# Kernel optimization log

Hardware: AMD Instinct MI355X
Metric: run time of the kernel (lower is better)

## Reference

```python
import jax, jax.numpy as jnp
import numpy as np

T, B, D, H = 1024, 64, 512, 512


def setup_inputs() -> dict:
    key = jax.random.key(0)
    ks = jax.random.split(key, 12)
    s_in = 1.0 / np.sqrt(D + H)  # torch Linear default init scale
    inp = {
        "inputs": jax.random.normal(ks[0], (T, B, D), dtype=jnp.float32),
        "Wf": jax.random.uniform(ks[1], (H, D + H), jnp.float32, -s_in, s_in),
        "bf": jax.random.uniform(ks[2], (H,), jnp.float32, -s_in, s_in),
        "Wi": jax.random.uniform(ks[3], (H, D + H), jnp.float32, -s_in, s_in),
        "bi": jax.random.uniform(ks[4], (H,), jnp.float32, -s_in, s_in),
        "Wg": jax.random.uniform(ks[5], (H, D + H), jnp.float32, -s_in, s_in),
        "bg": jax.random.uniform(ks[6], (H,), jnp.float32, -s_in, s_in),
        "Wo": jax.random.uniform(ks[7], (H, D + H), jnp.float32, -s_in, s_in),
        "bo": jax.random.uniform(ks[8], (H,), jnp.float32, -s_in, s_in),
        "q_scale": jnp.ones((H,), jnp.float32),
        "q_bias": jax.random.normal(ks[9], (H,), dtype=jnp.float32),
    }
    return inp


def reference(inputs, Wf, bf, Wi, bi, Wg, bg, Wo, bo, q_scale, q_bias):
    # Fuse the four gate projections into one GEMM: same math as 4 Linears.
    W_all = jnp.concatenate([Wf, Wi, Wg, Wo], axis=0)   # [4H, D+H]
    b_all = jnp.concatenate([bf, bi, bg, bo], axis=0)   # [4H]
    Bsz = inputs.shape[1]
    h0 = jnp.zeros((Bsz, H), inputs.dtype)
    c0 = jnp.zeros((Bsz, H), inputs.dtype)

    def qresc(a):
        return jnp.tanh(a * q_scale + q_bias)

    def step(carry, x):
        hx, cx = carry
        comb = jnp.concatenate([x, hx], axis=1)          # [B, D+H]
        z = comb @ W_all.T + b_all                       # [B, 4H]
        f, i, g, o = jnp.split(z, 4, axis=1)
        f = qresc(jax.nn.sigmoid(f))
        i = qresc(jax.nn.sigmoid(i))
        g = qresc(jnp.tanh(g))
        o = qresc(jax.nn.sigmoid(o))
        cx = f * cx + i * g
        hx = o * jnp.tanh(cx)
        return (hx, cx), hx

    (hx, cx), outputs = jax.lax.scan(step, (h0, c0), inputs)
    return outputs, hx, cx
```

## Files before the change

### kernel.cpp

```cpp
#include <hip/hip_runtime.h>


#define T_STEPS 1024
#define BATCH   64
#define DIM     512
#define HID     512
#define NGROUPS 4
#define BPG     64
#define BB      16
#define NBLOCKS 256

typedef __bf16 bf16_t;
typedef __bf16 bf16x8 __attribute__((ext_vector_type(8)));
typedef float  f32x4  __attribute__((ext_vector_type(4)));

#define WS_FLAGS_OFF 0
#define WS_WB_OFF    4096
#define WB_BYTES     ((size_t)64*32*1024*2)
#define WS_XB_OFF    (WS_WB_OFF + WB_BYTES)
#define XB_BYTES     ((size_t)T_STEPS*BATCH*DIM*2)
#define HBUF_BYTES   ((size_t)(T_STEPS+1)*BATCH*HID*2)
#define WS_FULL      (WS_XB_OFF + XB_BYTES + HBUF_BYTES)
#define WS_MIN       (WS_XB_OFF + HBUF_BYTES)

#define SMEM_BYTES 99328
#define LROW_W 1032
#define LROW_H 520

__device__ __forceinline__ unsigned pk2(float lo, float hi) {
  unsigned a = (unsigned)__builtin_bit_cast(unsigned short, (bf16_t)lo);
  unsigned b = (unsigned)__builtin_bit_cast(unsigned short, (bf16_t)hi);
  return (b << 16) | a;
}

__global__ void prep_kernel(const float* __restrict__ Wf, const float* __restrict__ Wi,
                            const float* __restrict__ Wg, const float* __restrict__ Wo,
                            const float* __restrict__ X,
                            unsigned* __restrict__ flags, unsigned* __restrict__ Wb,
                            unsigned* __restrict__ Xb, unsigned* __restrict__ hbuf0,
                            int hasXb) {
  size_t nthr = (size_t)gridDim.x * blockDim.x;
  size_t t0 = (size_t)blockIdx.x * blockDim.x + threadIdx.x;
  if (t0 < NBLOCKS) flags[t0] = 0u;
  for (size_t i = t0; i < (size_t)BATCH * HID / 2; i += nthr) hbuf0[i] = 0u;
  for (size_t i = t0; i < (size_t)64 * 32 * 512; i += nthr) {
    int j = (int)(i >> 14);
    int rem = (int)(i & 16383);
    int srow = rem >> 9, k2 = rem & 511;
    int wv = srow >> 4, cc = srow & 15, gg = cc & 3, hl = cc >> 2;
    int h = j * 8 + wv * 4 + hl;
    const float* W = (gg == 0) ? Wf : (gg == 1) ? Wi : (gg == 2) ? Wg : Wo;
    float f0 = W[(size_t)h * 1024 + 2 * (size_t)k2];
    float f1 = W[(size_t)h * 1024 + 2 * (size_t)k2 + 1];
    Wb[i] = pk2(f0, f1);
  }
  if (hasXb) {
    for (size_t i = t0; i < (size_t)T_STEPS * BATCH * DIM / 2; i += nthr)
      Xb[i] = pk2(X[2 * i], X[2 * i + 1]);
  }
}

__global__ __launch_bounds__(128, 1) void lstm_kernel(
    const float* __restrict__ X, const bf16_t* __restrict__ Xb, int hasXb,
    const float* __restrict__ bf_, const float* __restrict__ bi_,
    const float* __restrict__ bg_, const float* __restrict__ bo_,
    const float* __restrict__ qs_, const float* __restrict__ qb_,
    float* __restrict__ out, unsigned* __restrict__ flags,
    const bf16_t* __restrict__ Wb, bf16_t* __restrict__ hbuf) {

  extern __shared__ char smem[];
  bf16_t* Wsl = (bf16_t*)smem;
  bf16_t* hsh = (bf16_t*)(smem + 66048);
#define WSL(r, k)    Wsl[(r) * LROW_W + (k)]
#define HSH(b, r, k) hsh[(b) * (16 * LROW_H) + (r) * LROW_H + (k)]

  const int blk = blockIdx.x;
  const int g = blk >> 6, j = blk & 63;
  const int bo2 = g * BB;
  const int tid = threadIdx.x, wv = tid >> 6, l = tid & 63;
  const int c = l & 15, rg = l >> 4, kq = rg * 8;
  const int gate = c & 3, hl = c >> 2;
  const int hcol = j * 8 + wv * 4 + hl;
  const int brow = wv * 16 + c;

  {
    const uint4* src = (const uint4*)(Wb + (size_t)j * 32 * 1024);
#pragma unroll
    for (int ii = 0; ii < 32; ii++) {
      int idx = ii * 128 + tid;
      int sr = idx >> 7, k8 = idx & 127;
      *(uint4*)&WSL(sr, k8 * 8) = src[idx];
    }
  }
  const float* bsrc = (gate == 0) ? bf_ : (gate == 1) ? bi_ : (gate == 2) ? bg_ : bo_;
  const float bias = bsrc[hcol];
  const float qs = qs_[hcol], qb = qb_[hcol];
  float cst[4] = {0.f, 0.f, 0.f, 0.f};
  __syncthreads();

  unsigned* hb32 = (unsigned*)hbuf;
  const unsigned* fl = flags + g * 64;

  bf16x8 xf[16];
  auto load_x = [&](int sidx) {
    if (hasXb) {
      const bf16_t* xs = Xb + ((size_t)sidx * BATCH + bo2 + c) * DIM + kq;
#pragma unroll
      for (int kt = 0; kt < 16; kt++) xf[kt] = *(const bf16x8*)(xs + kt * 32);
    } else {
      const float* xs = X + ((size_t)sidx * BATCH + bo2 + c) * DIM + kq;
#pragma unroll
      for (int kt = 0; kt < 16; kt++) {
        const float4* p = (const float4*)(xs + kt * 32);
        float4 a = p[0], b = p[1];
        bf16x8 v;
        v[0] = (bf16_t)a.x; v[1] = (bf16_t)a.y; v[2] = (bf16_t)a.z; v[3] = (bf16_t)a.w;
        v[4] = (bf16_t)b.x; v[5] = (bf16_t)b.y; v[6] = (bf16_t)b.z; v[7] = (bf16_t)b.w;
        xf[kt] = v;
      }
    }
  };
  load_x(0);

  for (int s = 0; s < T_STEPS; s++) {
    const int buf = s & 1;
    {
      int cap = 0;
      while (true) {
        unsigned v = __hip_atomic_load(&fl[l], __ATOMIC_RELAXED, __HIP_MEMORY_SCOPE_AGENT);
        if (__all((int)(v >= (unsigned)s))) break;
        if (++cap > (1 << 20)) break;
      }
    }
    asm volatile("" ::: "memory");

    uint4 hreg[8];
    {
      const uint4* hs = (const uint4*)(hbuf + ((size_t)s * BATCH + bo2) * HID);
#pragma unroll
      for (int ii = 0; ii < 8; ii++) hreg[ii] = hs[ii * 128 + tid];
    }
    f32x4 acc = {bias, bias, bias, bias};
#pragma unroll
    for (int kt = 0; kt < 16; kt++) {
      bf16x8 b = *(const bf16x8*)&WSL(brow, kq + kt * 32);
      acc = __builtin_amdgcn_mfma_f32_16x16x32_bf16(xf[kt], b, acc, 0, 0, 0);
    }
#pragma unroll
    for (int ii = 0; ii < 8; ii++) {
      int idx = ii * 128 + tid;
      int r = idx >> 6, ch = idx & 63;
      *(uint4*)&HSH(buf, r, ch * 8) = hreg[ii];
    }
    __syncthreads();
#pragma unroll
    for (int kt = 0; kt < 16; kt++) {
      bf16x8 a = *(const bf16x8*)&HSH(buf, c, kq + kt * 32);
      bf16x8 b = *(const bf16x8*)&WSL(brow, 512 + kq + kt * 32);
      acc = __builtin_amdgcn_mfma_f32_16x16x32_bf16(a, b, acc, 0, 0, 0);
    }
    float hq[4];
#pragma unroll
    for (int q = 0; q < 4; q++) {
      float z = acc[q];
      float sg = 1.f / (1.f + __expf(-z));
      float th = 1.f - 2.f / (1.f + __expf(2.f * z));
      float a0 = (gate == 2) ? th : sg;
      float act = 1.f - 2.f / (1.f + __expf(2.f * (a0 * qs + qb)));
      float x1 = __shfl_xor(act, 1), x2 = __shfl_xor(act, 2), x3 = __shfl_xor(act, 3);
      float vf = (gate == 0) ? act : (gate == 1) ? x1 : (gate == 2) ? x2 : x3;
      float vi = (gate == 0) ? x1 : (gate == 1) ? act : (gate == 2) ? x3 : x2;
      float vg = (gate == 0) ? x2 : (gate == 1) ? x3 : (gate == 2) ? act : x1;
      float vo = (gate == 0) ? x3 : (gate == 1) ? x2 : (gate == 2) ? x1 : act;
      float cn = vf * cst[q] + vi * vg;
      cst[q] = cn;
      hq[q] = vo * (1.f - 2.f / (1.f + __expf(2.f * cn)));
    }
    float hp0 = __shfl_xor(hq[0], 4), hp1 = __shfl_xor(hq[1], 4);
    float hp2 = __shfl_xor(hq[2], 4), hp3 = __shfl_xor(hq[3], 4);
    if ((c & 7) == 0) {
      int m = c >> 3;
      size_t bi2 = (size_t)(s + 1) * (BATCH * HID / 2) +
                   (size_t)(bo2 + rg * 4) * (HID / 2) + (size_t)(j * 4 + wv * 2 + m);
      __hip_atomic_store(&hb32[bi2 + 0],   pk2(hq[0], hp0), __ATOMIC_RELAXED, __HIP_MEMORY_SCOPE_AGENT);
      __hip_atomic_store(&hb32[bi2 + 256], pk2(hq[1], hp1), __ATOMIC_RELAXED, __HIP_MEMORY_SCOPE_AGENT);
      __hip_atomic_store(&hb32[bi2 + 512], pk2(hq[2], hp2), __ATOMIC_RELAXED, __HIP_MEMORY_SCOPE_AGENT);
      __hip_atomic_store(&hb32[bi2 + 768], pk2(hq[3], hp3), __ATOMIC_RELAXED, __HIP_MEMORY_SCOPE_AGENT);
    }
    if (gate == 0) {
      size_t ob = ((size_t)s * BATCH + bo2 + rg * 4) * HID + hcol;
      out[ob] = hq[0]; out[ob + 512] = hq[1]; out[ob + 1024] = hq[2]; out[ob + 1536] = hq[3];
      if (s == T_STEPS - 1) {
        size_t hb = (size_t)T_STEPS * BATCH * HID + (size_t)(bo2 + rg * 4) * HID + hcol;
        size_t cb = hb + (size_t)BATCH * HID;
        out[hb] = hq[0]; out[hb + 512] = hq[1]; out[hb + 1024] = hq[2]; out[hb + 1536] = hq[3];
        out[cb] = cst[0]; out[cb + 512] = cst[1]; out[cb + 1024] = cst[2]; out[cb + 1536] = cst[3];
      }
    }
    asm volatile("" ::: "memory");
    load_x((s + 1 < T_STEPS) ? s + 1 : T_STEPS - 1);
    asm volatile("s_waitcnt vmcnt(16)" ::: "memory");
    __builtin_amdgcn_s_barrier();
    if (tid == 0)
      __hip_atomic_store(&flags[blk], (unsigned)(s + 1), __ATOMIC_RELAXED,
                         __HIP_MEMORY_SCOPE_AGENT);
  }
#undef WSL
#undef HSH
}

extern "C" void kernel_launch(void* const* d_in, const int* in_sizes, int n_in,
                              void* d_out, int out_size, void* d_ws, size_t ws_size,
                              hipStream_t stream) {
  const float* X  = (const float*)d_in[0];
  const float* Wf = (const float*)d_in[1];
  const float* bf = (const float*)d_in[2];
  const float* Wi = (const float*)d_in[3];
  const float* bi = (const float*)d_in[4];
  const float* Wg = (const float*)d_in[5];
  const float* bg = (const float*)d_in[6];
  const float* Wo = (const float*)d_in[7];
  const float* bo = (const float*)d_in[8];
  const float* qs = (const float*)d_in[9];
  const float* qb = (const float*)d_in[10];
  float* out = (float*)d_out;

  if (ws_size < WS_MIN) return;
  int hasXb = (ws_size >= WS_FULL) ? 1 : 0;

  char* ws = (char*)d_ws;
  unsigned* flags = (unsigned*)(ws + WS_FLAGS_OFF);
  bf16_t* Wb = (bf16_t*)(ws + WS_WB_OFF);
  bf16_t* Xb = (bf16_t*)(ws + WS_XB_OFF);
  bf16_t* hbuf = (bf16_t*)(ws + (hasXb ? (WS_XB_OFF + XB_BYTES) : WS_XB_OFF));

  hipLaunchKernelGGL(prep_kernel, dim3(4096), dim3(256), 0, stream,
                     Wf, Wi, Wg, Wo, X, flags, (unsigned*)Wb, (unsigned*)Xb,
                     (unsigned*)hbuf, hasXb);

  (void)hipFuncSetAttribute((const void*)lstm_kernel,
                            hipFuncAttributeMaxDynamicSharedMemorySize, SMEM_BYTES);

  const bf16_t* Xbc = Xb;
  const bf16_t* Wbc = Wb;
  void* args[] = {(void*)&X, (void*)&Xbc, (void*)&hasXb,
                  (void*)&bf, (void*)&bi, (void*)&bg, (void*)&bo,
                  (void*)&qs, (void*)&qb, (void*)&out, (void*)&flags,
                  (void*)&Wbc, (void*)&hbuf};
  hipLaunchCooperativeKernel((void*)lstm_kernel, dim3(NBLOCKS), dim3(128),
                             args, SMEM_BYTES, stream);
}
```

Measured before the change: 5.927 ms.

## Partition LSTM blocks by XCD so each batch group syncs within one die

Each block reads its XCC_ID at start and takes a slot from a per-XCD roster. When all eight XCDs hold exactly 32 blocks, each XCD owns eight batch rows and flag polling and h stores use only sc0 (L2-local) coherence, avoiding cross-die traffic. Blocks grow to 256 threads covering 16 hidden units, and h fragments load straight from global memory into registers, removing the LDS staging and one __syncthreads. The x-projection MFMAs are issued before the wait so they overlap it, and the X bf16 pre-conversion is dropped. Half of the MFMA rows now compute unused batch rows, and the fast path relies on an even block-to-XCD spread, otherwise it falls back to agent-scope atomics.

```diff
diff --git a/kernel.cpp b/kernel.cpp
--- a/kernel.cpp
+++ b/kernel.cpp
@@ -5,27 +5,27 @@
 #define BATCH   64
 #define DIM     512
 #define HID     512
-#define NGROUPS 4
-#define BPG     64
-#define BB      16
+#define KDIM    1024
 #define NBLOCKS 256
+#define TPB     256
+#define NXCD    8
+#define GSIZE   32
+#define GROWS   8
 
 typedef __bf16 bf16_t;
 typedef __bf16 bf16x8 __attribute__((ext_vector_type(8)));
 typedef float  f32x4  __attribute__((ext_vector_type(4)));
 
-#define WS_FLAGS_OFF 0
+#define WS_CTL_U32   272
 #define WS_WB_OFF    4096
-#define WB_BYTES     ((size_t)64*32*1024*2)
-#define WS_XB_OFF    (WS_WB_OFF + WB_BYTES)
-#define XB_BYTES     ((size_t)T_STEPS*BATCH*DIM*2)
-#define HBUF_BYTES   ((size_t)(T_STEPS+1)*BATCH*HID*2)
-#define WS_FULL      (WS_XB_OFF + XB_BYTES + HBUF_BYTES)
-#define WS_MIN       (WS_XB_OFF + HBUF_BYTES)
-
-#define SMEM_BYTES 99328
+#define WB_BYTES     ((size_t)32 * 64 * KDIM * 2)
+#define WS_HBUF_OFF  (WS_WB_OFF + WB_BYTES)
+#define HBUF_BYTES   ((size_t)(T_STEPS + 1) * BATCH * HID * 2)
+#define WS_REQUIRED  (WS_HBUF_OFF + HBUF_BYTES)
+
 #define LROW_W 1032
-#define LROW_H 520
+#define SMEM_W_BYTES (64 * LROW_W * 2)
+#define SMEM_BYTES   (SMEM_W_BYTES + 32)
 
 __device__ __forceinline__ unsigned pk2(float lo, float hi) {
   unsigned a = (unsigned)__builtin_bit_cast(unsigned short, (bf16_t)lo);
@@ -35,59 +35,74 @@
 
 __global__ void prep_kernel(const float* __restrict__ Wf, const float* __restrict__ Wi,
                             const float* __restrict__ Wg, const float* __restrict__ Wo,
-                            const float* __restrict__ X,
-                            unsigned* __restrict__ flags, unsigned* __restrict__ Wb,
-                            unsigned* __restrict__ Xb, unsigned* __restrict__ hbuf0,
-                            int hasXb) {
-  size_t nthr = (size_t)gridDim.x * blockDim.x;
-  size_t t0 = (size_t)blockIdx.x * blockDim.x + threadIdx.x;
-  if (t0 < NBLOCKS) flags[t0] = 0u;
-  for (size_t i = t0; i < (size_t)BATCH * HID / 2; i += nthr) hbuf0[i] = 0u;
-  for (size_t i = t0; i < (size_t)64 * 32 * 512; i += nthr) {
-    int j = (int)(i >> 14);
-    int rem = (int)(i & 16383);
-    int srow = rem >> 9, k2 = rem & 511;
-    int wv = srow >> 4, cc = srow & 15, gg = cc & 3, hl = cc >> 2;
-    int h = j * 8 + wv * 4 + hl;
+                            unsigned* __restrict__ ctl, unsigned* __restrict__ Wb,
+                            unsigned* __restrict__ hbuf0) {
+  unsigned i = blockIdx.x * 256 + threadIdx.x;
+  if (i < WS_CTL_U32) ctl[i] = 0u;
+  if (i < BATCH * HID / 2) hbuf0[i] = 0u;
+  if (i < 32u * 64u * 512u) {
+    int slot = (int)(i >> 15);
+    int rem = (int)(i & 32767);
+    int row = rem >> 9, k2 = rem & 511;
+    int w = row >> 4, cc = row & 15, gg = cc & 3, hl = cc >> 2;
+    int h = slot * 16 + w * 4 + hl;
     const float* W = (gg == 0) ? Wf : (gg == 1) ? Wi : (gg == 2) ? Wg : Wo;
-    float f0 = W[(size_t)h * 1024 + 2 * (size_t)k2];
-    float f1 = W[(size_t)h * 1024 + 2 * (size_t)k2 + 1];
+    float f0 = W[(size_t)h * KDIM + 2 * (size_t)k2];
+    float f1 = W[(size_t)h * KDIM + 2 * (size_t)k2 + 1];
     Wb[i] = pk2(f0, f1);
   }
-  if (hasXb) {
-    for (size_t i = t0; i < (size_t)T_STEPS * BATCH * DIM / 2; i += nthr)
-      Xb[i] = pk2(X[2 * i], X[2 * i + 1]);
-  }
-}
-
-__global__ __launch_bounds__(128, 1) void lstm_kernel(
-    const float* __restrict__ X, const bf16_t* __restrict__ Xb, int hasXb,
+}
+
+__global__ __launch_bounds__(TPB, 1) void lstm_kernel(
+    const float* __restrict__ X,
     const float* __restrict__ bf_, const float* __restrict__ bi_,
     const float* __restrict__ bg_, const float* __restrict__ bo_,
     const float* __restrict__ qs_, const float* __restrict__ qb_,
-    float* __restrict__ out, unsigned* __restrict__ flags,
+    float* __restrict__ out,
+    unsigned* __restrict__ flags, unsigned* __restrict__ roster,
+    unsigned* __restrict__ gctr,
     const bf16_t* __restrict__ Wb, bf16_t* __restrict__ hbuf) {
 
   extern __shared__ char smem[];
   bf16_t* Wsl = (bf16_t*)smem;
-  bf16_t* hsh = (bf16_t*)(smem + 66048);
-#define WSL(r, k)    Wsl[(r) * LROW_W + (k)]
-#define HSH(b, r, k) hsh[(b) * (16 * LROW_H) + (r) * LROW_H + (k)]
-
-  const int blk = blockIdx.x;
-  const int g = blk >> 6, j = blk & 63;
-  const int bo2 = g * BB;
-  const int tid = threadIdx.x, wv = tid >> 6, l = tid & 63;
+  int* comm = (int*)(smem + SMEM_W_BYTES);
+#define WSL(r, k) Wsl[(r) * LROW_W + (k)]
+
+  const int tid = threadIdx.x;
+  const int wv = tid >> 6, l = tid & 63;
   const int c = l & 15, rg = l >> 4, kq = rg * 8;
   const int gate = c & 3, hl = c >> 2;
-  const int hcol = j * 8 + wv * 4 + hl;
-  const int brow = wv * 16 + c;
+
+  if (tid == 0) {
+    unsigned xcc;
+    asm volatile("s_getreg_b32 %0, hwreg(HW_REG_XCC_ID)" : "=s"(xcc));
+    xcc &= 7u;
+    unsigned tk = __hip_atomic_fetch_add(&roster[xcc], 1u, __ATOMIC_RELAXED,
+                                         __HIP_MEMORY_SCOPE_AGENT);
+    __hip_atomic_fetch_add(gctr, 1u, __ATOMIC_ACQ_REL, __HIP_MEMORY_SCOPE_AGENT);
+    int cap = 0;
+    while (__hip_atomic_load(gctr, __ATOMIC_ACQUIRE, __HIP_MEMORY_SCOPE_AGENT) <
+           (unsigned)NBLOCKS)
+      if (++cap > (1 << 24)) break;
+    unsigned ok = 1;
+    for (int x = 0; x < NXCD; x++)
+      ok &= (__hip_atomic_load(&roster[x], __ATOMIC_RELAXED,
+                               __HIP_MEMORY_SCOPE_AGENT) == (unsigned)GSIZE);
+    comm[0] = (int)xcc; comm[1] = (int)tk; comm[2] = (int)ok;
+  }
+  __syncthreads();
+  const int xcdm = comm[2];
+  const int g    = xcdm ? comm[0] : ((int)blockIdx.x >> 5);
+  const int slot = xcdm ? comm[1] : ((int)blockIdx.x & 31);
+  const int bo   = g * GROWS;
+  const int hcol = slot * 16 + wv * 4 + hl;
+  const int myrow = bo + c;
 
   {
-    const uint4* src = (const uint4*)(Wb + (size_t)j * 32 * 1024);
+    const uint4* src = (const uint4*)(Wb + (size_t)slot * 64 * KDIM);
 #pragma unroll
     for (int ii = 0; ii < 32; ii++) {
-      int idx = ii * 128 + tid;
+      int idx = ii * TPB + tid;
       int sr = idx >> 7, k8 = idx & 127;
       *(uint4*)&WSL(sr, k8 * 8) = src[idx];
     }
@@ -96,26 +111,30 @@
   const float bias = bsrc[hcol];
   const float qs = qs_[hcol], qb = qb_[hcol];
   float cst[4] = {0.f, 0.f, 0.f, 0.f};
+  bf16x8 xf[16], hfr[16];
+  {
+    bf16x8 z;
+#pragma unroll
+    for (int i = 0; i < 8; i++) z[i] = (bf16_t)0.f;
+#pragma unroll
+    for (int i = 0; i < 16; i++) { xf[i] = z; hfr[i] = z; }
+  }
   __syncthreads();
 
   unsigned* hb32 = (unsigned*)hbuf;
-  const unsigned* fl = flags + g * 64;
-
-  bf16x8 xf[16];
+  const unsigned* fl = flags + g * GSIZE;
+  unsigned* myflag = flags + g * GSIZE + slot;
+
   auto load_x = [&](int sidx) {
-    if (hasXb) {
-      const bf16_t* xs = Xb + ((size_t)sidx * BATCH + bo2 + c) * DIM + kq;
-#pragma unroll
-      for (int kt = 0; kt < 16; kt++) xf[kt] = *(const bf16x8*)(xs + kt * 32);
-    } else {
-      const float* xs = X + ((size_t)sidx * BATCH + bo2 + c) * DIM + kq;
+    if (c < 8) {
+      const float* xs = X + ((size_t)sidx * BATCH + myrow) * DIM + kq;
 #pragma unroll
       for (int kt = 0; kt < 16; kt++) {
-        const float4* p = (const float4*)(xs + kt * 32);
-        float4 a = p[0], b = p[1];
+        float4 a4 = *(const float4*)(xs + kt * 32);
+        float4 b4 = *(const float4*)(xs + kt * 32 + 4);
         bf16x8 v;
-        v[0] = (bf16_t)a.x; v[1] = (bf16_t)a.y; v[2] = (bf16_t)a.z; v[3] = (bf16_t)a.w;
-        v[4] = (bf16_t)b.x; v[5] = (bf16_t)b.y; v[6] = (bf16_t)b.z; v[7] = (bf16_t)b.w;
+        v[0] = (bf16_t)a4.x; v[1] = (bf16_t)a4.y; v[2] = (bf16_t)a4.z; v[3] = (bf16_t)a4.w;
+        v[4] = (bf16_t)b4.x; v[5] = (bf16_t)b4.y; v[6] = (bf16_t)b4.z; v[7] = (bf16_t)b4.w;
         xf[kt] = v;
       }
     }
@@ -123,46 +142,53 @@
   load_x(0);
 
   for (int s = 0; s < T_STEPS; s++) {
-    const int buf = s & 1;
+    f32x4 accA1 = {bias, bias, bias, bias}, accA2 = {0.f, 0.f, 0.f, 0.f};
+#pragma unroll
+    for (int kt = 0; kt < 8; kt++) {
+      bf16x8 b = *(const bf16x8*)&WSL(wv * 16 + c, kq + kt * 32);
+      accA1 = __builtin_amdgcn_mfma_f32_16x16x32_bf16(xf[kt], b, accA1, 0, 0, 0);
+    }
+#pragma unroll
+    for (int kt = 8; kt < 16; kt++) {
+      bf16x8 b = *(const bf16x8*)&WSL(wv * 16 + c, kq + kt * 32);
+      accA2 = __builtin_amdgcn_mfma_f32_16x16x32_bf16(xf[kt], b, accA2, 0, 0, 0);
+    }
+    load_x((s + 1 < T_STEPS) ? s + 1 : s);
     {
+      const unsigned* fp = fl + (l & 31);
       int cap = 0;
       while (true) {
-        unsigned v = __hip_atomic_load(&fl[l], __ATOMIC_RELAXED, __HIP_MEMORY_SCOPE_AGENT);
+        unsigned v;
+        if (xcdm)
+          asm volatile("global_load_dword %0, %1, off sc0\n\ts_waitcnt vmcnt(0)"
+                       : "=v"(v) : "v"(fp) : "memory");
+        else
+          asm volatile("global_load_dword %0, %1, off sc0 sc1\n\ts_waitcnt vmcnt(0)"
+                       : "=v"(v) : "v"(fp) : "memory");
         if (__all((int)(v >= (unsigned)s))) break;
-        if (++cap > (1 << 20)) break;
-      }
-    }
-    asm volatile("" ::: "memory");
-
-    uint4 hreg[8];
-    {
-      const uint4* hs = (const uint4*)(hbuf + ((size_t)s * BATCH + bo2) * HID);
-#pragma unroll
-      for (int ii = 0; ii < 8; ii++) hreg[ii] = hs[ii * 128 + tid];
-    }
-    f32x4 acc = {bias, bias, bias, bias};
-#pragma unroll
-    for (int kt = 0; kt < 16; kt++) {
-      bf16x8 b = *(const bf16x8*)&WSL(brow, kq + kt * 32);
-      acc = __builtin_amdgcn_mfma_f32_16x16x32_bf16(xf[kt], b, acc, 0, 0, 0);
-    }
-#pragma unroll
-    for (int ii = 0; ii < 8; ii++) {
-      int idx = ii * 128 + tid;
-      int r = idx >> 6, ch = idx & 63;
-      *(uint4*)&HSH(buf, r, ch * 8) = hreg[ii];
-    }
-    __syncthreads();
-#pragma unroll
-    for (int kt = 0; kt < 16; kt++) {
-      bf16x8 a = *(const bf16x8*)&HSH(buf, c, kq + kt * 32);
-      bf16x8 b = *(const bf16x8*)&WSL(brow, 512 + kq + kt * 32);
-      acc = __builtin_amdgcn_mfma_f32_16x16x32_bf16(a, b, acc, 0, 0, 0);
+        if (++cap > (1 << 18)) break;
+      }
+    }
+    if (c < 8) {
+      const bf16_t* hrow = hbuf + ((size_t)s * BATCH + myrow) * HID + kq;
+#pragma unroll
+      for (int kt = 0; kt < 16; kt++) hfr[kt] = *(const bf16x8*)(hrow + kt * 32);
+    }
+    f32x4 acc1 = {0.f, 0.f, 0.f, 0.f}, acc2 = {0.f, 0.f, 0.f, 0.f};
+#pragma unroll
+    for (int kt = 0; kt < 8; kt++) {
+      bf16x8 b = *(const bf16x8*)&WSL(wv * 16 + c, 512 + kq + kt * 32);
+      acc1 = __builtin_amdgcn_mfma_f32_16x16x32_bf16(hfr[kt], b, acc1, 0, 0, 0);
+    }
+#pragma unroll
+    for (int kt = 8; kt < 16; kt++) {
+      bf16x8 b = *(const bf16x8*)&WSL(wv * 16 + c, 512 + kq + kt * 32);
+      acc2 = __builtin_amdgcn_mfma_f32_16x16x32_bf16(hfr[kt], b, acc2, 0, 0, 0);
     }
     float hq[4];
 #pragma unroll
     for (int q = 0; q < 4; q++) {
-      float z = acc[q];
+      float z = accA1[q] + accA2[q] + acc1[q] + acc2[q];
       float sg = 1.f / (1.f + __expf(-z));
       float th = 1.f - 2.f / (1.f + __expf(2.f * z));
       float a0 = (gate == 2) ? th : sg;
@@ -176,37 +202,47 @@
       cst[q] = cn;
       hq[q] = vo * (1.f - 2.f / (1.f + __expf(2.f * cn)));
     }
-    float hp0 = __shfl_xor(hq[0], 4), hp1 = __shfl_xor(hq[1], 4);
-    float hp2 = __shfl_xor(hq[2], 4), hp3 = __shfl_xor(hq[3], 4);
-    if ((c & 7) == 0) {
-      int m = c >> 3;
-      size_t bi2 = (size_t)(s + 1) * (BATCH * HID / 2) +
-                   (size_t)(bo2 + rg * 4) * (HID / 2) + (size_t)(j * 4 + wv * 2 + m);
-      __hip_atomic_store(&hb32[bi2 + 0],   pk2(hq[0], hp0), __ATOMIC_RELAXED, __HIP_MEMORY_SCOPE_AGENT);
-      __hip_atomic_store(&hb32[bi2 + 256], pk2(hq[1], hp1), __ATOMIC_RELAXED, __HIP_MEMORY_SCOPE_AGENT);
-      __hip_atomic_store(&hb32[bi2 + 512], pk2(hq[2], hp2), __ATOMIC_RELAXED, __HIP_MEMORY_SCOPE_AGENT);
-      __hip_atomic_store(&hb32[bi2 + 768], pk2(hq[3], hp3), __ATOMIC_RELAXED, __HIP_MEMORY_SCOPE_AGENT);
-    }
-    if (gate == 0) {
-      size_t ob = ((size_t)s * BATCH + bo2 + rg * 4) * HID + hcol;
-      out[ob] = hq[0]; out[ob + 512] = hq[1]; out[ob + 1024] = hq[2]; out[ob + 1536] = hq[3];
+#pragma unroll
+    for (int q = 0; q < 4; q++) {
+      float v4 = __shfl_xor(hq[q], 4);
+      unsigned a = pk2(hq[q], v4);
+      unsigned b = __shfl_xor(a, 8);
+      if (c == 0 && rg < 2) {
+        int row = bo + rg * 4 + q;
+        size_t idx = ((size_t)(s + 1) * BATCH + row) * (HID / 2) + slot * 8 + wv * 2;
+        if (xcdm) {
+          hb32[idx] = a; hb32[idx + 1] = b;
+        } else {
+          __hip_atomic_store(&hb32[idx], a, __ATOMIC_RELAXED, __HIP_MEMORY_SCOPE_AGENT);
+          __hip_atomic_store(&hb32[idx + 1], b, __ATOMIC_RELAXED, __HIP_MEMORY_SCOPE_AGENT);
+        }
+      }
+    }
+    if (gate == 0 && rg < 2) {
+      size_t ob = ((size_t)s * BATCH + bo + rg * 4) * HID + hcol;
+      out[ob] = hq[0]; out[ob + HID] = hq[1];
+      out[ob + 2 * HID] = hq[2]; out[ob + 3 * HID] = hq[3];
       if (s == T_STEPS - 1) {
-        size_t hb = (size_t)T_STEPS * BATCH * HID + (size_t)(bo2 + rg * 4) * HID + hcol;
+        size_t hb = (size_t)T_STEPS * BATCH * HID + (size_t)(bo + rg * 4) * HID + hcol;
         size_t cb = hb + (size_t)BATCH * HID;
-        out[hb] = hq[0]; out[hb + 512] = hq[1]; out[hb + 1024] = hq[2]; out[hb + 1536] = hq[3];
-        out[cb] = cst[0]; out[cb + 512] = cst[1]; out[cb + 1024] = cst[2]; out[cb + 1536] = cst[3];
-      }
-    }
+        out[hb] = hq[0]; out[hb + HID] = hq[1];
+        out[hb + 2 * HID] = hq[2]; out[hb + 3 * HID] = hq[3];
+        out[cb] = cst[0]; out[cb + HID] = cst[1];
+        out[cb + 2 * HID] = cst[2]; out[cb + 3 * HID] = cst[3];
+      }
+    }
+    asm volatile("s_waitcnt vmcnt(0)" ::: "memory");
+    __builtin_amdgcn_s_barrier();
     asm volatile("" ::: "memory");
-    load_x((s + 1 < T_STEPS) ? s + 1 : T_STEPS - 1);
-    asm volatile("s_waitcnt vmcnt(16)" ::: "memory");
-    __builtin_amdgcn_s_barrier();
-    if (tid == 0)
-      __hip_atomic_store(&flags[blk], (unsigned)(s + 1), __ATOMIC_RELAXED,
-                         __HIP_MEMORY_SCOPE_AGENT);
+    if (tid == 0) {
+      unsigned fv = (unsigned)(s + 1);
+      if (xcdm)
+        asm volatile("global_store_dword %0, %1, off sc0" :: "v"(myflag), "v"(fv) : "memory");
+      else
+        __hip_atomic_store(myflag, fv, __ATOMIC_RELAXED, __HIP_MEMORY_SCOPE_AGENT);
+    }
   }
 #undef WSL
-#undef HSH
 }
 
 extern "C" void kernel_launch(void* const* d_in, const int* in_sizes, int n_in,
@@ -225,28 +261,26 @@
   const float* qb = (const float*)d_in[10];
   float* out = (float*)d_out;
 
-  if (ws_size < WS_MIN) return;
-  int hasXb = (ws_size >= WS_FULL) ? 1 : 0;
+  if (ws_size < WS_REQUIRED) return;
 
   char* ws = (char*)d_ws;
-  unsigned* flags = (unsigned*)(ws + WS_FLAGS_OFF);
-  bf16_t* Wb = (bf16_t*)(ws + WS_WB_OFF);
-  bf16_t* Xb = (bf16_t*)(ws + WS_XB_OFF);
-  bf16_t* hbuf = (bf16_t*)(ws + (hasXb ? (WS_XB_OFF + XB_BYTES) : WS_XB_OFF));
+  unsigned* ctl    = (unsigned*)ws;
+  unsigned* flags  = ctl;
+  unsigned* roster = ctl + 256;
+  unsigned* gctr   = ctl + 264;
+  bf16_t* Wb   = (bf16_t*)(ws + WS_WB_OFF);
+  bf16_t* hbuf = (bf16_t*)(ws + WS_HBUF_OFF);
 
   hipLaunchKernelGGL(prep_kernel, dim3(4096), dim3(256), 0, stream,
-                     Wf, Wi, Wg, Wo, X, flags, (unsigned*)Wb, (unsigned*)Xb,
-                     (unsigned*)hbuf, hasXb);
+                     Wf, Wi, Wg, Wo, ctl, (unsigned*)Wb, (unsigned*)hbuf);
 
   (void)hipFuncSetAttribute((const void*)lstm_kernel,
                             hipFuncAttributeMaxDynamicSharedMemorySize, SMEM_BYTES);
 
-  const bf16_t* Xbc = Xb;
   const bf16_t* Wbc = Wb;
-  void* args[] = {(void*)&X, (void*)&Xbc, (void*)&hasXb,
-                  (void*)&bf, (void*)&bi, (void*)&bg, (void*)&bo,
+  void* args[] = {(void*)&X, (void*)&bf, (void*)&bi, (void*)&bg, (void*)&bo,
                   (void*)&qs, (void*)&qb, (void*)&out, (void*)&flags,
-                  (void*)&Wbc, (void*)&hbuf};
-  hipLaunchCooperativeKernel((void*)lstm_kernel, dim3(NBLOCKS), dim3(128),
+                  (void*)&roster, (void*)&gctr, (void*)&Wbc, (void*)&hbuf};
+  hipLaunchCooperativeKernel((void*)lstm_kernel, dim3(NBLOCKS), dim3(TPB),
                              args, SMEM_BYTES, stream);
 }
```

New measurement: 6.225 ms. +5.0%, slower.
